# Performance work log

Measured on AMD Instinct MI355X. Metric: run time of the kernel, lower is better.

## Reference

```python
import jax, jax.numpy as jnp
import numpy as np

B, T, F, H, A, D = 1024, 256, 128, 128, 8, 256


def setup_inputs() -> dict:
    key = jax.random.key(0)
    ks = jax.random.split(key, 16)
    s = lambda k, shape, scale: jax.random.normal(k, shape, dtype=jnp.float32) * scale
    return {
        "h": jax.random.normal(ks[0], (B, T, F), dtype=jnp.float32),
        # LSTM params (flax LSTMCell: input kernel no bias, hidden kernel with bias; gate order i,f,g,o)
        "Wx": s(ks[1], (F, 4 * H), 1.0 / np.sqrt(F)),
        "Wh": s(ks[2], (H, 4 * H), 1.0 / np.sqrt(H)),
        "bh": jnp.zeros((4 * H,), jnp.float32),
        # actor head
        "Wa1": s(ks[3], (H, D), np.sqrt(2.0 / H)),
        "ba1": jnp.zeros((D,), jnp.float32),
        "Wa2": s(ks[4], (D, D), np.sqrt(2.0 / D)),
        "ba2": jnp.zeros((D,), jnp.float32),
        "Wa3": s(ks[5], (D, A), 0.01 / np.sqrt(D)),
        "ba3": jnp.zeros((A,), jnp.float32),
        "log_std": jnp.zeros((A,), jnp.float32),
        # critic head
        "Wc1": s(ks[6], (H, D), np.sqrt(2.0 / H)),
        "bc1": jnp.zeros((D,), jnp.float32),
        "Wc2": s(ks[7], (D, D), np.sqrt(2.0 / D)),
        "bc2": jnp.zeros((D,), jnp.float32),
        "Wc3": s(ks[8], (D, 1), 1.0 / np.sqrt(D)),
        "bc3": jnp.zeros((1,), jnp.float32),
    }


def reference(h, Wx, Wh, bh, Wa1, ba1, Wa2, ba2, Wa3, ba3, log_std,
              Wc1, bc1, Wc2, bc2, Wc3, bc3):
    act = jnp.tanh  # activation='tanh'
    # Precompute input projections for all gates: [B,T,4H] -> scan over time.
    xg = jnp.einsum('btf,fg->btg', h, Wx)
    c0 = jnp.zeros((h.shape[0], H), h.dtype)
    h0 = jnp.zeros((h.shape[0], H), h.dtype)

    def step(carry, xg_t):
        c, hs = carry
        z = xg_t + hs @ Wh + bh  # [B,4H]
        i = jax.nn.sigmoid(z[:, :H])
        f = jax.nn.sigmoid(z[:, H:2 * H])
        g = jnp.tanh(z[:, 2 * H:3 * H])
        o = jax.nn.sigmoid(z[:, 3 * H:])
        c = f * c + i * g
        hs = o * jnp.tanh(c)
        return (c, hs), None

    (_, x), _ = jax.lax.scan(step, (c0, h0), jnp.swapaxes(xg, 0, 1))  # x = last hidden [B,H]

    a = act(x @ Wa1 + ba1)
    a = act(a @ Wa2 + ba2)
    mean = a @ Wa3 + ba3                      # [B,A] policy mean
    std = jnp.exp(log_std)                    # [A] policy std (diag)

    v = act(x @ Wc1 + bc1)
    v = act(v @ Wc2 + bc2)
    value = (v @ Wc3 + bc3)                   # [B,1]

    # Pack (mean, std, value) as in (pi, critic): [B, 2A+1]
    return jnp.concatenate([mean, jnp.broadcast_to(std, mean.shape), value], axis=-1)
```

## Files before the change

kernel.cpp:

```cpp
#include <hip/hip_runtime.h>


typedef _Float16 f16x8 __attribute__((ext_vector_type(8)));
typedef _Float16 f16x4 __attribute__((ext_vector_type(4)));
typedef float    f32x4 __attribute__((ext_vector_type(4)));

#define NLOG2E (-1.4426950408889634f)

__device__ __forceinline__ float rcpf(float x) { return __builtin_amdgcn_rcpf(x); }
__device__ __forceinline__ float ex2(float x)  { return __builtin_amdgcn_exp2f(x); }

__device__ __forceinline__ f16x4 pack4(const float4 a) {
    f16x4 v;
    v[0] = (_Float16)a.x; v[1] = (_Float16)a.y;
    v[2] = (_Float16)a.z; v[3] = (_Float16)a.w;
    return v;
}

__global__ __launch_bounds__(512, 2)
void ac_fused(const float* __restrict__ hin,
              const float* __restrict__ Wx, const float* __restrict__ Wh,
              const float* __restrict__ bh,
              const float* __restrict__ Wa1, const float* __restrict__ ba1,
              const float* __restrict__ Wa2, const float* __restrict__ ba2,
              const float* __restrict__ Wa3, const float* __restrict__ ba3,
              const float* __restrict__ logstd,
              const float* __restrict__ Wc1, const float* __restrict__ bc1,
              const float* __restrict__ Wc2, const float* __restrict__ bc2,
              const float* __restrict__ Wc3, const float* __restrict__ bc3,
              float* __restrict__ out)
{
    constexpr int T = 256, F = 128, H = 128, G = 512;

    __shared__ f16x8 Hbuf[2][16][4];
    __shared__ f16x8 Axg[2][256];
    __shared__ float xf[4][F + 1];
    __shared__ float hb[2][4][257];
    __shared__ float redA[4][8][8];
    __shared__ float redC[4][32];

    const int tid  = threadIdx.x;
    const int lane = tid & 63;
    const int wv   = tid >> 6;
    const int m16  = lane & 15;
    const int q    = lane >> 4;
    const int r0   = blockIdx.x << 2;
    const int ncol = (wv << 4) + m16;

    f16x8 bwx[4][4], bwh[4][4];
    #pragma unroll
    for (int kt = 0; kt < 4; ++kt) {
        #pragma unroll
        for (int s = 0; s < 4; ++s) {
            f16x8 vx, vh;
            #pragma unroll
            for (int j = 0; j < 8; ++j) {
                const int k = (kt << 5) + (q << 3) + j;
                vx[j] = (_Float16)Wx[k * G + s * H + ncol];
                vh[j] = (_Float16)Wh[k * G + s * H + ncol];
            }
            bwx[s][kt] = vx;
            bwh[s][kt] = vh;
        }
    }
    const float nbi = NLOG2E * bh[0 * H + ncol];
    const float nbf = NLOG2E * bh[1 * H + ncol];
    const float nbg = 2.0f * NLOG2E * bh[2 * H + ncol];
    const float nbo = NLOG2E * bh[3 * H + ncol];

    const int xc = tid >> 1;
    const int xh = tid & 1;
    const int xk0 = ((xc >> 6) << 5) + (((xc >> 4) & 3) << 3) + (xh << 2);
    const float* pgbase = hin + (size_t)(r0 + ((xc >> 2) & 3)) * T * F
                              + (size_t)(xc & 3) * F + xk0;

    const int hr0 = (q << 2) + (m16 >> 2);
    const int hw  = ((((ncol >> 3) << 2) + q) << 3) + (ncol & 7);

    if (tid < 128) {
        f16x8 zz = {};
        ((f16x8*)Hbuf)[tid] = zz;
    }

    {
        const float4 xp0 = *(const float4*)(pgbase);
        const float4 xp1 = *(const float4*)(pgbase + 4 * (size_t)F);
        __syncthreads();
        *(f16x4*)((_Float16*)&Axg[0][0] + xc * 8 + xh * 4) = pack4(xp0);
        *(f16x4*)((_Float16*)&Axg[1][0] + xc * 8 + xh * 4) = pack4(xp1);
    }
    asm volatile("s_waitcnt lgkmcnt(0)" ::: "memory");
    __builtin_amdgcn_s_barrier();

    float cstate = 0.0f;
    float hcur   = 0.0f;

    for (int t0 = 0; t0 < T; t0 += 8) {
        f32x4 P[2][4];
        #pragma unroll
        for (int mt = 0; mt < 2; ++mt)
            #pragma unroll
            for (int s = 0; s < 4; ++s) P[mt][s] = f32x4{0.f, 0.f, 0.f, 0.f};
        #pragma unroll
        for (int kt = 0; kt < 4; ++kt) {
            const f16x8 fr0 = Axg[0][(kt << 6) + lane];
            const f16x8 fr1 = Axg[1][(kt << 6) + lane];
            P[0][0] = __builtin_amdgcn_mfma_f32_16x16x32_f16(fr0, bwx[0][kt], P[0][0], 0, 0, 0);
            P[0][1] = __builtin_amdgcn_mfma_f32_16x16x32_f16(fr0, bwx[1][kt], P[0][1], 0, 0, 0);
            P[0][2] = __builtin_amdgcn_mfma_f32_16x16x32_f16(fr0, bwx[2][kt], P[0][2], 0, 0, 0);
            P[0][3] = __builtin_amdgcn_mfma_f32_16x16x32_f16(fr0, bwx[3][kt], P[0][3], 0, 0, 0);
            P[1][0] = __builtin_amdgcn_mfma_f32_16x16x32_f16(fr1, bwx[0][kt], P[1][0], 0, 0, 0);
            P[1][1] = __builtin_amdgcn_mfma_f32_16x16x32_f16(fr1, bwx[1][kt], P[1][1], 0, 0, 0);
            P[1][2] = __builtin_amdgcn_mfma_f32_16x16x32_f16(fr1, bwx[2][kt], P[1][2], 0, 0, 0);
            P[1][3] = __builtin_amdgcn_mfma_f32_16x16x32_f16(fr1, bwx[3][kt], P[1][3], 0, 0, 0);
        }

        float4 xp0n, xp1n;
        #pragma unroll
        for (int i = 0; i < 8; ++i) {
            const int t = t0 + i;
            const f16x8* Hc = &Hbuf[t & 1][0][0];
            _Float16*    Hn = (_Float16*)&Hbuf[(t + 1) & 1][0][0];

            if (i == 2) {
                const int t0n = (t0 + 8 < T) ? t0 + 8 : t0;
                xp0n = *(const float4*)(pgbase + (size_t)t0n * F);
                xp1n = *(const float4*)(pgbase + (size_t)(t0n + 4) * F);
            }

            const f16x8 af0 = Hc[hr0];
            const f16x8 af1 = Hc[16 + hr0];
            const f16x8 af2 = Hc[32 + hr0];
            const f16x8 af3 = Hc[48 + hr0];

            const int mt = i >> 2, rg = i & 3;
            const float x0 = P[mt][0][rg], x1 = P[mt][1][rg];
            const float x2 = P[mt][2][rg], x3 = P[mt][3][rg];
            f32x4 a0 = {x0, x0, x0, x0}, a1 = {x1, x1, x1, x1};
            f32x4 a2 = {x2, x2, x2, x2}, a3 = {x3, x3, x3, x3};

            a0 = __builtin_amdgcn_mfma_f32_16x16x32_f16(af0, bwh[0][0], a0, 0, 0, 0);
            a1 = __builtin_amdgcn_mfma_f32_16x16x32_f16(af0, bwh[1][0], a1, 0, 0, 0);
            a2 = __builtin_amdgcn_mfma_f32_16x16x32_f16(af0, bwh[2][0], a2, 0, 0, 0);
            a3 = __builtin_amdgcn_mfma_f32_16x16x32_f16(af0, bwh[3][0], a3, 0, 0, 0);
            a0 = __builtin_amdgcn_mfma_f32_16x16x32_f16(af1, bwh[0][1], a0, 0, 0, 0);
            a1 = __builtin_amdgcn_mfma_f32_16x16x32_f16(af1, bwh[1][1], a1, 0, 0, 0);
            a2 = __builtin_amdgcn_mfma_f32_16x16x32_f16(af1, bwh[2][1], a2, 0, 0, 0);
            a3 = __builtin_amdgcn_mfma_f32_16x16x32_f16(af1, bwh[3][1], a3, 0, 0, 0);
            a0 = __builtin_amdgcn_mfma_f32_16x16x32_f16(af2, bwh[0][2], a0, 0, 0, 0);
            a1 = __builtin_amdgcn_mfma_f32_16x16x32_f16(af2, bwh[1][2], a1, 0, 0, 0);
            a2 = __builtin_amdgcn_mfma_f32_16x16x32_f16(af2, bwh[2][2], a2, 0, 0, 0);
            a3 = __builtin_amdgcn_mfma_f32_16x16x32_f16(af2, bwh[3][2], a3, 0, 0, 0);
            a0 = __builtin_amdgcn_mfma_f32_16x16x32_f16(af3, bwh[0][3], a0, 0, 0, 0);
            a1 = __builtin_amdgcn_mfma_f32_16x16x32_f16(af3, bwh[1][3], a1, 0, 0, 0);
            a2 = __builtin_amdgcn_mfma_f32_16x16x32_f16(af3, bwh[2][3], a2, 0, 0, 0);
            a3 = __builtin_amdgcn_mfma_f32_16x16x32_f16(af3, bwh[3][3], a3, 0, 0, 0);

            const float iv = rcpf(1.0f + ex2(fmaf(a0[0], NLOG2E, nbi)));
            const float fv = rcpf(1.0f + ex2(fmaf(a1[0], NLOG2E, nbf)));
            const float gv = 2.0f * rcpf(1.0f + ex2(fmaf(a2[0], 2.0f * NLOG2E, nbg))) - 1.0f;
            const float ov = rcpf(1.0f + ex2(fmaf(a3[0], NLOG2E, nbo)));
            cstate = fv * cstate + iv * gv;
            const float th = 2.0f * rcpf(1.0f + ex2(cstate * (2.0f * NLOG2E))) - 1.0f;
            hcur = ov * th;

            Hn[hw] = (_Float16)hcur;

            if (i == 7) {
                *(f16x4*)((_Float16*)&Axg[0][0] + xc * 8 + xh * 4) = pack4(xp0n);
                *(f16x4*)((_Float16*)&Axg[1][0] + xc * 8 + xh * 4) = pack4(xp1n);
            }

            asm volatile("s_waitcnt lgkmcnt(0)" ::: "memory");
            __builtin_amdgcn_s_barrier();
        }
    }

    xf[q][ncol] = hcur;
    __syncthreads();

    const int n  = tid & 255;
    const int rh = tid >> 8;

    auto tanhl = [&](float x) { return 2.0f * rcpf(1.0f + ex2(x * (2.0f * NLOG2E))) - 1.0f; };

    auto layer = [&](const float* __restrict__ W, const float* __restrict__ bv,
                     const float* xin, int xs, int K, float* yout, int ys) {
        float acc0, acc1;
        const float b = bv[n];
        acc0 = b; acc1 = b;
        #pragma unroll 16
        for (int k = 0; k < K; ++k) {
            const float w = W[k * 256 + n];
            acc0 += xin[(rh * 2 + 0) * xs + k] * w;
            acc1 += xin[(rh * 2 + 1) * xs + k] * w;
        }
        yout[(rh * 2 + 0) * ys + n] = tanhl(acc0);
        yout[(rh * 2 + 1) * ys + n] = tanhl(acc1);
    };

    layer(Wa1, ba1, &xf[0][0], F + 1, 128, &hb[0][0][0], 257);
    __syncthreads();
    layer(Wa2, ba2, &hb[0][0][0], 257, 256, &hb[1][0][0], 257);
    __syncthreads();
    layer(Wc1, bc1, &xf[0][0], F + 1, 128, &hb[0][0][0], 257);
    if (tid < 256) {
        const int r = tid >> 6, aa = (tid >> 3) & 7, seg = tid & 7;
        float acc = 0.0f;
        const int k0 = seg << 5;
        #pragma unroll 16
        for (int k = k0; k < k0 + 32; ++k) acc += hb[1][r][k] * Wa3[k * 8 + aa];
        redA[r][aa][seg] = acc;
    }
    __syncthreads();
    layer(Wc2, bc2, &hb[0][0][0], 257, 256, &hb[1][0][0], 257);
    if (tid < 32) {
        const int r = tid >> 3, aa = tid & 7;
        float acc = ba3[aa];
        #pragma unroll
        for (int s = 0; s < 8; ++s) acc += redA[r][aa][s];
        out[(size_t)(r0 + r) * 17 + aa]     = acc;
        out[(size_t)(r0 + r) * 17 + 8 + aa] = __expf(logstd[aa]);
    }
    __syncthreads();
    if (tid < 128) {
        const int r = tid >> 5, seg = tid & 31;
        float acc = 0.0f;
        const int k0 = seg << 3;
        #pragma unroll
        for (int k = k0; k < k0 + 8; ++k) acc += hb[1][r][k] * Wc3[k];
        redC[r][seg] = acc;
    }
    __syncthreads();
    if (tid < 4) {
        float acc = bc3[0];
        #pragma unroll
        for (int s = 0; s < 32; ++s) acc += redC[tid][s];
        out[(size_t)(r0 + tid) * 17 + 16] = acc;
    }
}

extern "C" void kernel_launch(void* const* d_in, const int* in_sizes, int n_in,
                              void* d_out, int out_size, void* d_ws, size_t ws_size,
                              hipStream_t stream) {
    (void)in_sizes; (void)n_in; (void)d_ws; (void)ws_size; (void)out_size;
    const float* hin = (const float*)d_in[0];
    const float* Wx  = (const float*)d_in[1];
    const float* Wh  = (const float*)d_in[2];
    const float* bh  = (const float*)d_in[3];
    const float* Wa1 = (const float*)d_in[4];
    const float* ba1 = (const float*)d_in[5];
    const float* Wa2 = (const float*)d_in[6];
    const float* ba2 = (const float*)d_in[7];
    const float* Wa3 = (const float*)d_in[8];
    const float* ba3 = (const float*)d_in[9];
    const float* ls  = (const float*)d_in[10];
    const float* Wc1 = (const float*)d_in[11];
    const float* bc1 = (const float*)d_in[12];
    const float* Wc2 = (const float*)d_in[13];
    const float* bc2 = (const float*)d_in[14];
    const float* Wc3 = (const float*)d_in[15];
    const float* bc3 = (const float*)d_in[16];

    hipLaunchKernelGGL(ac_fused, dim3(256), dim3(512), 0, stream,
                       hin, Wx, Wh, bh, Wa1, ba1, Wa2, ba2, Wa3, ba3, ls,
                       Wc1, bc1, Wc2, bc2, Wc3, bc3, (float*)d_out);
}
```

Measured before the change: 348.9 us.

## Pre-scale input gate projections and run actor and critic heads concurrently

```diff
diff --git a/kernel.cpp b/kernel.cpp
--- a/kernel.cpp
+++ b/kernel.cpp
@@ -35,7 +35,8 @@
     __shared__ f16x8 Hbuf[2][16][4];
     __shared__ f16x8 Axg[2][256];
     __shared__ float xf[4][F + 1];
-    __shared__ float hb[2][4][257];
+    __shared__ float hb1[2][4][257];
+    __shared__ float hb2[2][4][257];
     __shared__ float redA[4][8][8];
     __shared__ float redC[4][32];
 
@@ -68,6 +69,8 @@
     const float nbg = 2.0f * NLOG2E * bh[2 * H + ncol];
     const float nbo = NLOG2E * bh[3 * H + ncol];
 
+    const f32x4 zq = {0.f, 0.f, 0.f, 0.f};
+
     const int xc = tid >> 1;
     const int xh = tid & 1;
     const int xk0 = ((xc >> 6) << 5) + (((xc >> 4) & 3) << 3) + (xh << 2);
@@ -97,12 +100,20 @@
 
     for (int t0 = 0; t0 < T; t0 += 8) {
         f32x4 P[2][4];
-        #pragma unroll
-        for (int mt = 0; mt < 2; ++mt)
-            #pragma unroll
-            for (int s = 0; s < 4; ++s) P[mt][s] = f32x4{0.f, 0.f, 0.f, 0.f};
-        #pragma unroll
-        for (int kt = 0; kt < 4; ++kt) {
+        {
+            const f16x8 fr0 = Axg[0][lane];
+            const f16x8 fr1 = Axg[1][lane];
+            P[0][0] = __builtin_amdgcn_mfma_f32_16x16x32_f16(fr0, bwx[0][0], zq, 0, 0, 0);
+            P[0][1] = __builtin_amdgcn_mfma_f32_16x16x32_f16(fr0, bwx[1][0], zq, 0, 0, 0);
+            P[0][2] = __builtin_amdgcn_mfma_f32_16x16x32_f16(fr0, bwx[2][0], zq, 0, 0, 0);
+            P[0][3] = __builtin_amdgcn_mfma_f32_16x16x32_f16(fr0, bwx[3][0], zq, 0, 0, 0);
+            P[1][0] = __builtin_amdgcn_mfma_f32_16x16x32_f16(fr1, bwx[0][0], zq, 0, 0, 0);
+            P[1][1] = __builtin_amdgcn_mfma_f32_16x16x32_f16(fr1, bwx[1][0], zq, 0, 0, 0);
+            P[1][2] = __builtin_amdgcn_mfma_f32_16x16x32_f16(fr1, bwx[2][0], zq, 0, 0, 0);
+            P[1][3] = __builtin_amdgcn_mfma_f32_16x16x32_f16(fr1, bwx[3][0], zq, 0, 0, 0);
+        }
+        #pragma unroll
+        for (int kt = 1; kt < 4; ++kt) {
             const f16x8 fr0 = Axg[0][(kt << 6) + lane];
             const f16x8 fr1 = Axg[1][(kt << 6) + lane];
             P[0][0] = __builtin_amdgcn_mfma_f32_16x16x32_f16(fr0, bwx[0][kt], P[0][0], 0, 0, 0);
@@ -114,6 +125,16 @@
             P[1][2] = __builtin_amdgcn_mfma_f32_16x16x32_f16(fr1, bwx[2][kt], P[1][2], 0, 0, 0);
             P[1][3] = __builtin_amdgcn_mfma_f32_16x16x32_f16(fr1, bwx[3][kt], P[1][3], 0, 0, 0);
         }
+        #pragma unroll
+        for (int mt = 0; mt < 2; ++mt) {
+            #pragma unroll
+            for (int g = 0; g < 4; ++g) {
+                P[mt][0][g] = fmaf(P[mt][0][g], NLOG2E,        nbi);
+                P[mt][1][g] = fmaf(P[mt][1][g], NLOG2E,        nbf);
+                P[mt][2][g] = fmaf(P[mt][2][g], 2.0f * NLOG2E, nbg);
+                P[mt][3][g] = fmaf(P[mt][3][g], NLOG2E,        nbo);
+            }
+        }
 
         float4 xp0n, xp1n;
         #pragma unroll
@@ -122,27 +143,21 @@
             const f16x8* Hc = &Hbuf[t & 1][0][0];
             _Float16*    Hn = (_Float16*)&Hbuf[(t + 1) & 1][0][0];
 
+            const f16x8 af0 = Hc[hr0];
+            const f16x8 af1 = Hc[16 + hr0];
+            const f16x8 af2 = Hc[32 + hr0];
+            const f16x8 af3 = Hc[48 + hr0];
+
             if (i == 2) {
                 const int t0n = (t0 + 8 < T) ? t0 + 8 : t0;
                 xp0n = *(const float4*)(pgbase + (size_t)t0n * F);
                 xp1n = *(const float4*)(pgbase + (size_t)(t0n + 4) * F);
             }
 
-            const f16x8 af0 = Hc[hr0];
-            const f16x8 af1 = Hc[16 + hr0];
-            const f16x8 af2 = Hc[32 + hr0];
-            const f16x8 af3 = Hc[48 + hr0];
-
-            const int mt = i >> 2, rg = i & 3;
-            const float x0 = P[mt][0][rg], x1 = P[mt][1][rg];
-            const float x2 = P[mt][2][rg], x3 = P[mt][3][rg];
-            f32x4 a0 = {x0, x0, x0, x0}, a1 = {x1, x1, x1, x1};
-            f32x4 a2 = {x2, x2, x2, x2}, a3 = {x3, x3, x3, x3};
-
-            a0 = __builtin_amdgcn_mfma_f32_16x16x32_f16(af0, bwh[0][0], a0, 0, 0, 0);
-            a1 = __builtin_amdgcn_mfma_f32_16x16x32_f16(af0, bwh[1][0], a1, 0, 0, 0);
-            a2 = __builtin_amdgcn_mfma_f32_16x16x32_f16(af0, bwh[2][0], a2, 0, 0, 0);
-            a3 = __builtin_amdgcn_mfma_f32_16x16x32_f16(af0, bwh[3][0], a3, 0, 0, 0);
+            f32x4 a0 = __builtin_amdgcn_mfma_f32_16x16x32_f16(af0, bwh[0][0], zq, 0, 0, 0);
+            f32x4 a1 = __builtin_amdgcn_mfma_f32_16x16x32_f16(af0, bwh[1][0], zq, 0, 0, 0);
+            f32x4 a2 = __builtin_amdgcn_mfma_f32_16x16x32_f16(af0, bwh[2][0], zq, 0, 0, 0);
+            f32x4 a3 = __builtin_amdgcn_mfma_f32_16x16x32_f16(af0, bwh[3][0], zq, 0, 0, 0);
             a0 = __builtin_amdgcn_mfma_f32_16x16x32_f16(af1, bwh[0][1], a0, 0, 0, 0);
             a1 = __builtin_amdgcn_mfma_f32_16x16x32_f16(af1, bwh[1][1], a1, 0, 0, 0);
             a2 = __builtin_amdgcn_mfma_f32_16x16x32_f16(af1, bwh[2][1], a2, 0, 0, 0);
@@ -156,10 +171,11 @@
             a2 = __builtin_amdgcn_mfma_f32_16x16x32_f16(af3, bwh[2][3], a2, 0, 0, 0);
             a3 = __builtin_amdgcn_mfma_f32_16x16x32_f16(af3, bwh[3][3], a3, 0, 0, 0);
 
-            const float iv = rcpf(1.0f + ex2(fmaf(a0[0], NLOG2E, nbi)));
-            const float fv = rcpf(1.0f + ex2(fmaf(a1[0], NLOG2E, nbf)));
-            const float gv = 2.0f * rcpf(1.0f + ex2(fmaf(a2[0], 2.0f * NLOG2E, nbg))) - 1.0f;
-            const float ov = rcpf(1.0f + ex2(fmaf(a3[0], NLOG2E, nbo)));
+            const int mt = i >> 2, rg = i & 3;
+            const float iv = rcpf(1.0f + ex2(fmaf(a0[0], NLOG2E,        P[mt][0][rg])));
+            const float fv = rcpf(1.0f + ex2(fmaf(a1[0], NLOG2E,        P[mt][1][rg])));
+            const float gv = 2.0f * rcpf(1.0f + ex2(fmaf(a2[0], 2.0f * NLOG2E, P[mt][2][rg]))) - 1.0f;
+            const float ov = rcpf(1.0f + ex2(fmaf(a3[0], NLOG2E,        P[mt][3][rg])));
             cstate = fv * cstate + iv * gv;
             const float th = 2.0f * rcpf(1.0f + ex2(cstate * (2.0f * NLOG2E))) - 1.0f;
             hcur = ov * th;
@@ -179,41 +195,60 @@
     xf[q][ncol] = hcur;
     __syncthreads();
 
-    const int n  = tid & 255;
-    const int rh = tid >> 8;
+    const int half = tid >> 8;
+    const int n    = tid & 255;
+    const float* W1 = half ? Wc1 : Wa1;
+    const float* b1 = half ? bc1 : ba1;
+    const float* W2 = half ? Wc2 : Wa2;
+    const float* b2 = half ? bc2 : ba2;
 
     auto tanhl = [&](float x) { return 2.0f * rcpf(1.0f + ex2(x * (2.0f * NLOG2E))) - 1.0f; };
 
-    auto layer = [&](const float* __restrict__ W, const float* __restrict__ bv,
-                     const float* xin, int xs, int K, float* yout, int ys) {
-        float acc0, acc1;
-        const float b = bv[n];
-        acc0 = b; acc1 = b;
+    {
+        float a0, a1, a2, a3;
+        const float b = b1[n];
+        a0 = a1 = a2 = a3 = b;
         #pragma unroll 16
-        for (int k = 0; k < K; ++k) {
-            const float w = W[k * 256 + n];
-            acc0 += xin[(rh * 2 + 0) * xs + k] * w;
-            acc1 += xin[(rh * 2 + 1) * xs + k] * w;
-        }
-        yout[(rh * 2 + 0) * ys + n] = tanhl(acc0);
-        yout[(rh * 2 + 1) * ys + n] = tanhl(acc1);
-    };
-
-    layer(Wa1, ba1, &xf[0][0], F + 1, 128, &hb[0][0][0], 257);
-    __syncthreads();
-    layer(Wa2, ba2, &hb[0][0][0], 257, 256, &hb[1][0][0], 257);
-    __syncthreads();
-    layer(Wc1, bc1, &xf[0][0], F + 1, 128, &hb[0][0][0], 257);
+        for (int k = 0; k < 128; ++k) {
+            const float w = W1[k * 256 + n];
+            a0 += xf[0][k] * w; a1 += xf[1][k] * w;
+            a2 += xf[2][k] * w; a3 += xf[3][k] * w;
+        }
+        hb1[half][0][n] = tanhl(a0); hb1[half][1][n] = tanhl(a1);
+        hb1[half][2][n] = tanhl(a2); hb1[half][3][n] = tanhl(a3);
+    }
+    __syncthreads();
+    {
+        float a0, a1, a2, a3;
+        const float b = b2[n];
+        a0 = a1 = a2 = a3 = b;
+        #pragma unroll 16
+        for (int k = 0; k < 256; ++k) {
+            const float w = W2[k * 256 + n];
+            a0 += hb1[half][0][k] * w; a1 += hb1[half][1][k] * w;
+            a2 += hb1[half][2][k] * w; a3 += hb1[half][3][k] * w;
+        }
+        hb2[half][0][n] = tanhl(a0); hb2[half][1][n] = tanhl(a1);
+        hb2[half][2][n] = tanhl(a2); hb2[half][3][n] = tanhl(a3);
+    }
+    __syncthreads();
     if (tid < 256) {
         const int r = tid >> 6, aa = (tid >> 3) & 7, seg = tid & 7;
         float acc = 0.0f;
         const int k0 = seg << 5;
         #pragma unroll 16
-        for (int k = k0; k < k0 + 32; ++k) acc += hb[1][r][k] * Wa3[k * 8 + aa];
+        for (int k = k0; k < k0 + 32; ++k) acc += hb2[0][r][k] * Wa3[k * 8 + aa];
         redA[r][aa][seg] = acc;
-    }
-    __syncthreads();
-    layer(Wc2, bc2, &hb[0][0][0], 257, 256, &hb[1][0][0], 257);
+    } else if (tid < 384) {
+        const int u = tid - 256;
+        const int r = u >> 5, seg = u & 31;
+        float acc = 0.0f;
+        const int k0 = seg << 3;
+        #pragma unroll
+        for (int k = k0; k < k0 + 8; ++k) acc += hb2[1][r][k] * Wc3[k];
+        redC[r][seg] = acc;
+    }
+    __syncthreads();
     if (tid < 32) {
         const int r = tid >> 3, aa = tid & 7;
         float acc = ba3[aa];
@@ -221,22 +256,12 @@
         for (int s = 0; s < 8; ++s) acc += redA[r][aa][s];
         out[(size_t)(r0 + r) * 17 + aa]     = acc;
         out[(size_t)(r0 + r) * 17 + 8 + aa] = __expf(logstd[aa]);
-    }
-    __syncthreads();
-    if (tid < 128) {
-        const int r = tid >> 5, seg = tid & 31;
-        float acc = 0.0f;
-        const int k0 = seg << 3;
-        #pragma unroll
-        for (int k = k0; k < k0 + 8; ++k) acc += hb[1][r][k] * Wc3[k];
-        redC[r][seg] = acc;
-    }
-    __syncthreads();
-    if (tid < 4) {
+    } else if (tid >= 64 && tid < 68) {
+        const int r = tid - 64;
         float acc = bc3[0];
         #pragma unroll
-        for (int s = 0; s < 32; ++s) acc += redC[tid][s];
-        out[(size_t)(r0 + tid) * 17 + 16] = acc;
+        for (int s = 0; s < 32; ++s) acc += redC[r][s];
+        out[(size_t)(r0 + r) * 17 + 16] = acc;
     }
 }
 
```

Measured after the change: 342.2 us. About the same (-1.9%).
